# Kernel optimization log

Hardware: AMD Instinct MI355X
Metric: run time of the kernel (lower is better)

## Reference

```python
import jax, jax.numpy as jnp
import numpy as np

D_MODEL = 1024
NUM_HEADS = 16
HEAD_DIM = D_MODEL // NUM_HEADS  # 64
M_BITS = 32
B, N = 4, 2048


def setup_inputs() -> dict:
    key = jax.random.key(0)
    ks = jax.random.split(key, 6)
    s = 1.0 / np.sqrt(D_MODEL)
    se = 1.0 / np.sqrt(HEAD_DIM)
    return {
        "x": jax.random.normal(ks[0], (B, N, D_MODEL), dtype=jnp.float32),
        "Wq": jax.random.normal(ks[1], (D_MODEL, D_MODEL), dtype=jnp.float32) * s,
        "Wk": jax.random.normal(ks[2], (D_MODEL, D_MODEL), dtype=jnp.float32) * s,
        "Wv": jax.random.normal(ks[3], (D_MODEL, D_MODEL), dtype=jnp.float32) * s,
        # per-head witness (bit) encoders: project head_dim -> m_bits
        "W_enc": jax.random.normal(ks[4], (NUM_HEADS, HEAD_DIM, M_BITS), dtype=jnp.float32) * se,
        "Wo": jax.random.normal(ks[5], (D_MODEL, D_MODEL), dtype=jnp.float32) * s,
    }


def reference(x, Wq, Wk, Wv, W_enc, Wo):
    Bsz, Nq, _ = x.shape
    # QKV projections (nn.Linear, no bias): y = x @ W^T
    Q = x @ Wq.T
    K = x @ Wk.T  # self-attention: context = x
    V = x @ Wv.T
    # split heads: [B, N, H, hd]
    Qh = Q.reshape(Bsz, Nq, NUM_HEADS, HEAD_DIM)
    Kh = K.reshape(Bsz, Nq, NUM_HEADS, HEAD_DIM)
    Vh = V.reshape(Bsz, Nq, NUM_HEADS, HEAD_DIM)
    # witness encodings: soft-bit (tanh of random-hyperplane projections), m_bits << head_dim feature space
    q_enc = jnp.tanh(jnp.einsum("bnhd,hdm->bnhm", Qh, W_enc))
    k_enc = jnp.tanh(jnp.einsum("bnhd,hdm->bnhm", Kh, W_enc))
    # witness similarity scores over m_bits instead of full head_dim
    scale = 1.0 / np.sqrt(M_BITS)
    scores = jnp.einsum("bnhm,bkhm->bhnk", q_enc, k_enc) * scale  # [B,H,N,N]
    attn = jax.nn.softmax(scores, axis=-1)
    out = jnp.einsum("bhnk,bkhd->bnhd", attn, Vh).reshape(Bsz, Nq, D_MODEL)
    return out @ Wo.T
```

## Files before the change

### kernel.cpp

```cpp
#include <hip/hip_runtime.h>

typedef unsigned short u16;
typedef unsigned int u32;

typedef __bf16 bfrag __attribute__((ext_vector_type(8)));
typedef float f32x4 __attribute__((ext_vector_type(4)));
typedef float f32x16 __attribute__((ext_vector_type(16)));
typedef float f32x2 __attribute__((ext_vector_type(2)));

__device__ __forceinline__ float b2f(u16 h) {
    u32 u = ((u32)h) << 16;
    return __builtin_bit_cast(float, u);
}
__device__ __forceinline__ u16 f2b(float f) {
    u32 u = __builtin_bit_cast(u32, f);
    u += 0x7fffu + ((u >> 16) & 1u);
    return (u16)(u >> 16);
}
__device__ __forceinline__ u32 cvtpk(float lo, float hi) {
    u32 r;
    asm("v_cvt_pk_bf16_f32 %0, %1, %2" : "=v"(r) : "v"(lo), "v"(hi));
    return r;
}

#if defined(__has_builtin)
#if __has_builtin(__builtin_amdgcn_exp2f)
#define EXP2(x) __builtin_amdgcn_exp2f(x)
#endif
#endif
#ifndef EXP2
#define EXP2(x) exp2f(x)
#endif

#if defined(__has_builtin)
#if __has_builtin(__builtin_amdgcn_global_load_lds)
#define HAS_GLL 1
#endif
#endif
#ifndef HAS_GLL
#define HAS_GLL 0
#endif

#if HAS_GLL
typedef __attribute__((address_space(1))) const u32 as1_u32;
typedef __attribute__((address_space(3))) u32 as3_u32;
__device__ __forceinline__ void gl_lds16(const u16* g, u16* l) {
    __builtin_amdgcn_global_load_lds((as1_u32*)g, (as3_u32*)l, 16, 0, 0);
}
#endif

#if defined(__has_builtin)
#if __has_builtin(__builtin_amdgcn_permlane32_swap)
#define HAS_PLS 1
#endif
#endif
#ifndef HAS_PLS
#define HAS_PLS 0
#endif

__device__ __forceinline__ void plswap(u32 a, u32 b, u32& o0, u32& o1) {
#if HAS_PLS
    auto r = __builtin_amdgcn_permlane32_swap((int)a, (int)b, false, false);
    o0 = (u32)r[0];
    o1 = (u32)r[1];
#else
    int idx = ((int)(threadIdx.x & 63) ^ 32) << 2;
    u32 ca = (u32)__builtin_amdgcn_ds_bpermute(idx, (int)a);
    u32 cb = (u32)__builtin_amdgcn_ds_bpermute(idx, (int)b);
    bool hi = (threadIdx.x & 63) >= 32;
    o0 = hi ? cb : a;
    o1 = hi ? b : ca;
#endif
}

__device__ __forceinline__ void xcd_swizzle(int& bxn, int& bym) {
    int gx = gridDim.x;
    int nwg = gx * gridDim.y;
    int orig = blockIdx.x + gx * blockIdx.y;
    int nid = orig;
    if ((nwg & 7) == 0) {
        int cpx = nwg >> 3;
        nid = (orig & 7) * cpx + (orig >> 3);
    }
    bxn = nid % gx;
    bym = nid / gx;
}

#define BATCH 4
#define SEQ   2048
#define DM    1024
#define NH    16
#define HD    64
#define MB    32
#define STOK  (BATCH * SEQ)

#define QSCALE 0.25503524337503433f
#define TWOLOG2E 2.8853900817779268f

__device__ __forceinline__ void storeC(u16* C, size_t idx, float v)   { C[idx] = f2b(v); }
__device__ __forceinline__ void storeC(float* C, size_t idx, float v) { C[idx] = v; }

__global__ __launch_bounds__(256) void cvt3_f32_bf16(
    const float* __restrict__ a, const float* __restrict__ b,
    const float* __restrict__ c,
    u16* __restrict__ da, u16* __restrict__ db, u16* __restrict__ dc,
    int n8a, int n8bc)
{
    const int job = blockIdx.y;
    const float* s = (job == 0) ? a : ((job == 1) ? b : c);
    u16* d = (job == 0) ? da : ((job == 1) ? db : dc);
    int n8 = (job == 0) ? n8a : n8bc;
    int i = blockIdx.x * 256 + threadIdx.x;
    if (i >= n8) return;
    const float4* sp = (const float4*)s + (size_t)i * 2;
    float4 x = sp[0], y = sp[1];
    u16 t[8] = { f2b(x.x), f2b(x.y), f2b(x.z), f2b(x.w),
                 f2b(y.x), f2b(y.y), f2b(y.z), f2b(y.w) };
    ((uint4*)d)[i] = *(uint4*)t;
}

__global__ __launch_bounds__(256) void build_cqk(
    const float* __restrict__ Wq, const float* __restrict__ Wk,
    const float* __restrict__ Wenc, u16* __restrict__ CqkT)
{
    const int dblk = blockIdx.x;
    const int qk   = blockIdx.y >> 4;
    const int h    = blockIdx.y & 15;
    const float* W = qk ? Wk : Wq;
    __shared__ float we[64][32];
    const int tid = threadIdx.x;

    for (int p = 0; p < 8; ++p) {
        int idx = p * 256 + tid;
        we[idx >> 5][idx & 31] = Wenc[(size_t)h * (HD * MB) + idx];
    }
    __syncthreads();

    const int mh = tid >> 7;
    const int d  = dblk * 128 + (tid & 127);
    float acc[16] = {};
    for (int dh = 0; dh < 64; ++dh) {
        float w = W[(size_t)(h * 64 + dh) * DM + d];
        for (int m = 0; m < 16; ++m)
            acc[m] += w * we[dh][mh * 16 + m];
    }
    u16* dst = CqkT + (size_t)(qk * 512 + h * 32 + mh * 16) * DM + d;
    for (int m = 0; m < 16; ++m)
        dst[(size_t)m * DM] = f2b(acc[m]);
}

template <int TBM, typename TC>
__global__ __launch_bounds__(256) void gemm_bt(
    const u16* __restrict__ A, const u16* __restrict__ Bt, TC* __restrict__ C,
    int M, int Nc, int K)
{
    constexpr int FI = TBM / 32;
    __shared__ alignas(16) u16 As[TBM * 32];
    __shared__ alignas(16) u16 Bs[128 * 32];

    const int tid  = threadIdx.x;
    const int wave = tid >> 6;
    const int lane = tid & 63;
    const int quad = lane >> 4;
    const int lrow = lane & 15;
    int bxn, bym;
    xcd_swizzle(bxn, bym);
    const int bm = bym * TBM;
    const int bn = bxn * 128;
    const int wm = (wave & 1) * (TBM / 2);
    const int wn = (wave >> 1) * 64;

    f32x4 acc[FI][4] = {};

    for (int k0 = 0; k0 < K; k0 += 32) {
#if HAS_GLL
        for (int p = 0; p < TBM / 64; ++p) {
            int cbase = wave * TBM + p * 64;
            int cme   = cbase + lane;
            int row = cme >> 2, col = (cme & 3) * 8;
            gl_lds16(&A[(size_t)(bm + row) * K + k0 + col], &As[(size_t)cbase * 8]);
        }
        for (int p = 0; p < 2; ++p) {
            int cbase = wave * 128 + p * 64;
            int cme   = cbase + lane;
            int row = cme >> 2, col = (cme & 3) * 8;
            gl_lds16(&Bt[(size_t)(bn + row) * K + k0 + col], &Bs[(size_t)cbase * 8]);
        }
#else
        for (int p = 0; p < TBM / 64; ++p) {
            int idx = p * 256 + tid, row = idx >> 2, col = (idx & 3) * 8;
            *(uint4*)&As[row * 32 + col] = *(const uint4*)&A[(size_t)(bm + row) * K + k0 + col];
        }
        for (int p = 0; p < 2; ++p) {
            int idx = p * 256 + tid, row = idx >> 2, col = (idx & 3) * 8;
            *(uint4*)&Bs[row * 32 + col] = *(const uint4*)&Bt[(size_t)(bn + row) * K + k0 + col];
        }
#endif
        __syncthreads();

        bfrag af[FI], bfv[4];
        for (int i = 0; i < FI; ++i)
            af[i] = *(const bfrag*)&As[(wm + i * 16 + lrow) * 32 + quad * 8];
        for (int j = 0; j < 4; ++j)
            bfv[j] = *(const bfrag*)&Bs[(wn + j * 16 + lrow) * 32 + quad * 8];

        for (int i = 0; i < FI; ++i)
            for (int j = 0; j < 4; ++j)
                acc[i][j] = __builtin_amdgcn_mfma_f32_16x16x32_bf16(af[i], bfv[j], acc[i][j], 0, 0, 0);
        __syncthreads();
    }

    for (int i = 0; i < FI; ++i)
        for (int j = 0; j < 4; ++j)
            for (int r = 0; r < 4; ++r) {
                int row = bm + wm + i * 16 + quad * 4 + r;
                int col = bn + wn + j * 16 + lrow;
                storeC(C, (size_t)row * Nc + col, acc[i][j][r]);
            }
}

__global__ __launch_bounds__(256) void gemm_encv(
    const u16* __restrict__ A, const u16* __restrict__ Bt,
    u16* __restrict__ qe, u16* __restrict__ ke, u16* __restrict__ Vt)
{
    __shared__ alignas(16) u16 As[128 * 32];
    __shared__ alignas(16) u16 Bs[128 * 32];

    const int tid  = threadIdx.x;
    const int wave = tid >> 6;
    const int lane = tid & 63;
    const int quad = lane >> 4;
    const int lrow = lane & 15;
    int bxn, bym;
    xcd_swizzle(bxn, bym);
    const int bm = bym * 128;
    const int bn = bxn * 128;
    const int wm = (wave & 1) * 64;
    const int wn = (wave >> 1) * 64;

    f32x4 acc[4][4] = {};

    for (int k0 = 0; k0 < DM; k0 += 32) {
#if HAS_GLL
        for (int p = 0; p < 2; ++p) {
            int cbase = wave * 128 + p * 64;
            int cme   = cbase + lane;
            int row = cme >> 2, col = (cme & 3) * 8;
            gl_lds16(&A[(size_t)(bm + row) * DM + k0 + col], &As[(size_t)cbase * 8]);
            gl_lds16(&Bt[(size_t)(bn + row) * DM + k0 + col], &Bs[(size_t)cbase * 8]);
        }
#else
        for (int p = 0; p < 2; ++p) {
            int idx = p * 256 + tid, row = idx >> 2, col = (idx & 3) * 8;
            *(uint4*)&As[row * 32 + col] = *(const uint4*)&A[(size_t)(bm + row) * DM + k0 + col];
            *(uint4*)&Bs[row * 32 + col] = *(const uint4*)&Bt[(size_t)(bn + row) * DM + k0 + col];
        }
#endif
        __syncthreads();

        bfrag af[4], bfv[4];
        for (int i = 0; i < 4; ++i)
            af[i] = *(const bfrag*)&As[(wm + i * 16 + lrow) * 32 + quad * 8];
        for (int j = 0; j < 4; ++j)
            bfv[j] = *(const bfrag*)&Bs[(wn + j * 16 + lrow) * 32 + quad * 8];

        for (int i = 0; i < 4; ++i)
            for (int j = 0; j < 4; ++j)
                acc[i][j] = __builtin_amdgcn_mfma_f32_16x16x32_bf16(af[i], bfv[j], acc[i][j], 0, 0, 0);
        __syncthreads();
    }

    if (bn < 1024) {
        for (int i = 0; i < 4; ++i)
            for (int j = 0; j < 4; ++j) {
                int col = bn + wn + j * 16 + lrow;
                int hh = (col >> 5) & 15;
                int mm = col & 31;
                u16* dst = (col < 512) ? qe : ke;
                float qs = (col < 512) ? QSCALE : 1.0f;
                for (int r = 0; r < 4; ++r) {
                    int row = bm + wm + i * 16 + quad * 4 + r;
                    int bb = row >> 11, nn = row & 2047;
                    float e = EXP2(acc[i][j][r] * TWOLOG2E);
                    float t = (1.f - 2.f / (e + 1.f)) * qs;
                    dst[((size_t)(bb * NH + hh) * SEQ + nn) * MB + mm] = f2b(t);
                }
            }
    } else {
        for (int i = 0; i < 4; ++i)
            for (int j = 0; j < 4; ++j) {
                int col = bn - 1024 + wn + j * 16 + lrow;
                int hh = col >> 6, dd = col & 63;
                int row0 = bm + wm + i * 16 + quad * 4;
                int bb = row0 >> 11, nn = row0 & 2047;
                u16 t4[4] = { f2b(acc[i][j][0]), f2b(acc[i][j][1]),
                              f2b(acc[i][j][2]), f2b(acc[i][j][3]) };
                *(uint2*)&Vt[((size_t)(bb * NH + hh) * HD + dd) * SEQ + nn] = *(uint2*)t4;
            }
    }
}

__global__ __launch_bounds__(256, 4) void flash_attn(
    const u16* __restrict__ qe,
    const u16* __restrict__ ke,
    const u16* __restrict__ Vt,
    u16* __restrict__ AO)
{
    const int h = blockIdx.x, b = blockIdx.y, qt = blockIdx.z;
    const int tid  = threadIdx.x;
    const int wave = tid >> 6;
    const int lane = tid & 63;
    const int r31  = lane & 31;
    const int hi   = lane >> 5;

    __shared__ alignas(16) u16 Kt[2][64 * 32];
    __shared__ alignas(16) u16 Vtile[2][64 * 64];

    const size_t bhh = (size_t)(b * NH + h);
    const u16* keb = ke + bhh * SEQ * MB;
    const u16* qeb = qe + bhh * SEQ * MB;
    const u16* vtb = Vt + bhh * HD * SEQ;

    const int q0w = qt * 128 + wave * 32;

    const int klr = tid >> 2;
    const int ksl = tid & 3;
    const u16* ksrc = keb + (size_t)klr * MB + ((ksl ^ (klr & 3)) * 8);
    const int d0 = wave * 8 + (lane >> 3);
    const int c0 = lane & 7;
    const int g0 = (c0 ^ (d0 & 7)) * 8;
    const u16* vsrc0 = vtb + (size_t)d0 * SEQ + g0;
    const u16* vsrc1 = vtb + (size_t)(d0 + 32) * SEQ + g0;

#if HAS_GLL
    gl_lds16(ksrc,  Kt[0] + wave * 512);
    gl_lds16(vsrc0, Vtile[0] + wave * 512);
    gl_lds16(vsrc1, Vtile[0] + 2048 + wave * 512);
#else
    *(uint4*)&Kt[0][klr * 32 + ksl * 8] = *(const uint4*)ksrc;
    *(uint4*)&Vtile[0][d0 * 64 + c0 * 8] = *(const uint4*)vsrc0;
    *(uint4*)&Vtile[0][(d0 + 32) * 64 + c0 * 8] = *(const uint4*)vsrc1;
#endif
    ksrc += 64 * MB;
    vsrc0 += 64;
    vsrc1 += 64;

    bfrag qf[2];
    {
        const u16* qrow = qeb + (size_t)(q0w + r31) * MB;
        qf[0] = *(const bfrag*)&qrow[hi * 8];
        qf[1] = *(const bfrag*)&qrow[16 + hi * 8];
    }

    const f32x16 zero16 = {};

    f32x16 Oa[2] = {};
    f32x2 dacc = {0.f, 0.f};
    const int ksw = r31 & 3;
    const int vsw = r31 & 7;

    for (int c = 0; c < 32; ++c) {
        const int cur = c & 1, nxt = cur ^ 1;
        __syncthreads();

        if (c + 1 < 32) {
#if HAS_GLL
            gl_lds16(ksrc,  Kt[nxt] + wave * 512);
            gl_lds16(vsrc0, Vtile[nxt] + wave * 512);
            gl_lds16(vsrc1, Vtile[nxt] + 2048 + wave * 512);
#else
            *(uint4*)&Kt[nxt][klr * 32 + ksl * 8] = *(const uint4*)ksrc;
            *(uint4*)&Vtile[nxt][d0 * 64 + c0 * 8] = *(const uint4*)vsrc0;
            *(uint4*)&Vtile[nxt][(d0 + 32) * 64 + c0 * 8] = *(const uint4*)vsrc1;
#endif
            ksrc += 64 * MB;
            vsrc0 += 64;
            vsrc1 += 64;
        }

        const u16* KtC = Kt[cur];
        const u16* VtC = Vtile[cur];

        bfrag kf[2][2];
        for (int kt = 0; kt < 2; ++kt) {
            const u16* krow = &KtC[(kt * 32 + r31) * 32];
            kf[kt][0] = *(const bfrag*)&krow[((hi    ) ^ ksw) * 8];
            kf[kt][1] = *(const bfrag*)&krow[((2 + hi) ^ ksw) * 8];
        }

        bfrag pf[2][2];
        for (int kt = 0; kt < 2; ++kt) {
            __builtin_amdgcn_s_setprio(1);
            f32x16 St = __builtin_amdgcn_mfma_f32_32x32x16_bf16(kf[kt][0], qf[0], zero16, 0, 0, 0);
            St = __builtin_amdgcn_mfma_f32_32x32x16_bf16(kf[kt][1], qf[1], St, 0, 0, 0);
            __builtin_amdgcn_s_setprio(0);
            for (int kc = 0; kc < 2; ++kc) {
                float e0 = EXP2(St[8 * kc + 0]);
                float e1 = EXP2(St[8 * kc + 1]);
                float e2 = EXP2(St[8 * kc + 2]);
                float e3 = EXP2(St[8 * kc + 3]);
                float e4 = EXP2(St[8 * kc + 4]);
                float e5 = EXP2(St[8 * kc + 5]);
                float e6 = EXP2(St[8 * kc + 6]);
                float e7 = EXP2(St[8 * kc + 7]);
                f32x2 p0 = {e0, e1}, p1 = {e2, e3}, p2 = {e4, e5}, p3 = {e6, e7};
                dacc += (p0 + p1) + (p2 + p3);
                u32 A0 = cvtpk(e0, e1), A1 = cvtpk(e2, e3);
                u32 B0 = cvtpk(e4, e5), B1 = cvtpk(e6, e7);
                u32 w0, w1, w2, w3;
                plswap(A0, B0, w0, w2);
                plswap(A1, B1, w1, w3);
                uint4 words = { w0, w1, w2, w3 };
                pf[kt][kc] = __builtin_bit_cast(bfrag, words);
            }
        }

        __builtin_amdgcn_s_setprio(1);
        for (int dt = 0; dt < 2; ++dt) {
            const u16* vrow = &VtC[(dt * 32 + r31) * 64];
            for (int kt = 0; kt < 2; ++kt)
                for (int kc = 0; kc < 2; ++kc) {
                    bfrag vf = *(const bfrag*)&vrow[(((kt * 4 + kc * 2 + hi) ^ vsw) * 8)];
                    Oa[dt] = __builtin_amdgcn_mfma_f32_32x32x16_bf16(vf, pf[kt][kc], Oa[dt], 0, 0, 0);
                }
        }
        __builtin_amdgcn_s_setprio(0);
    }

    float dsum = dacc[0] + dacc[1];
    u32 o0, o1;
    plswap(__builtin_bit_cast(u32, dsum), __builtin_bit_cast(u32, dsum), o0, o1);
    float den = __builtin_bit_cast(float, o0) + __builtin_bit_cast(float, o1);

    {
        float inv = 1.0f / den;
        u16* aob = AO + (size_t)(b * SEQ + q0w + r31) * DM + h * HD;
        for (int dt = 0; dt < 2; ++dt)
            for (int g = 0; g < 4; ++g) {
                u16 t4[4] = { f2b(Oa[dt][g * 4 + 0] * inv),
                              f2b(Oa[dt][g * 4 + 1] * inv),
                              f2b(Oa[dt][g * 4 + 2] * inv),
                              f2b(Oa[dt][g * 4 + 3] * inv) };
                *(uint2*)&aob[dt * 32 + g * 8 + hi * 4] = *(uint2*)t4;
            }
    }
}

extern "C" void kernel_launch(void* const* d_in, const int* in_sizes, int n_in,
                              void* d_out, int out_size, void* d_ws, size_t ws_size,
                              hipStream_t stream) {
    const float* x    = (const float*)d_in[0];
    const float* Wq   = (const float*)d_in[1];
    const float* Wk   = (const float*)d_in[2];
    const float* Wv   = (const float*)d_in[3];
    const float* Wenc = (const float*)d_in[4];
    const float* Wo   = (const float*)d_in[5];
    float* out = (float*)d_out;

    const size_t MB1 = (size_t)1024 * 1024;
    char* ws = (char*)d_ws;
    u16* AO   = (u16*)(ws);
    u16* Wo_b = (u16*)(ws + 16 * MB1);
    u16* Bc   = (u16*)(ws + 18 * MB1);
    u16* Vt   = (u16*)(ws + 24 * MB1);
    u16* qe   = (u16*)(ws + 48 * MB1);
    u16* ke   = (u16*)(ws + 56 * MB1);

    u16* xb = (u16*)d_out;
    u16* wvb = Bc + (size_t)1024 * DM;

    cvt3_f32_bf16<<<dim3(STOK * DM / 8 / 256, 3), 256, 0, stream>>>(
        x, Wv, Wo, xb, wvb, Wo_b, STOK * DM / 8, DM * DM / 8);
    build_cqk<<<dim3(8, 32), 256, 0, stream>>>(Wq, Wk, Wenc, Bc);

    gemm_encv<<<dim3(2048 / 128, STOK / 128), 256, 0, stream>>>(xb, Bc, qe, ke, Vt);

    flash_attn<<<dim3(NH, BATCH, SEQ / 128), 256, 0, stream>>>(qe, ke, Vt, AO);

    gemm_bt<64, float><<<dim3(DM / 128, STOK / 64), 256, 0, stream>>>(AO, Wo_b, out, STOK, DM, DM);
}
```

Measured before the change: 251.5 us.

## Shrink flash attention blocks to two waves and 32-key tiles

Restructures the attention kernel so each block has 2 waves covering 64 queries instead of 4 waves covering 128, and iterates over 32-key chunks (64 iterations) instead of 64-key chunks. The K and V shared-memory tiles are halved and the V load/swizzle pattern now matches the K layout. The aim is lower register and LDS pressure per block, more blocks in flight, and a shorter softmax-to-MFMA dependency per iteration. The cost is twice as many barriers and K/V tile loads per query, and K/V reuse across queries within a block is halved.

```diff
diff --git a/kernel.cpp b/kernel.cpp
--- a/kernel.cpp
+++ b/kernel.cpp
@@ -300,7 +300,28 @@
     }
 }
 
-__global__ __launch_bounds__(256, 4) void flash_attn(
+__device__ __forceinline__ bfrag pack_half(const f32x16& St, int kc, f32x2& dacc)
+{
+    float e0 = EXP2(St[8 * kc + 0]);
+    float e1 = EXP2(St[8 * kc + 1]);
+    float e2 = EXP2(St[8 * kc + 2]);
+    float e3 = EXP2(St[8 * kc + 3]);
+    float e4 = EXP2(St[8 * kc + 4]);
+    float e5 = EXP2(St[8 * kc + 5]);
+    float e6 = EXP2(St[8 * kc + 6]);
+    float e7 = EXP2(St[8 * kc + 7]);
+    f32x2 p0 = {e0, e1}, p1 = {e2, e3}, p2 = {e4, e5}, p3 = {e6, e7};
+    dacc += (p0 + p1) + (p2 + p3);
+    u32 A0 = cvtpk(e0, e1), A1 = cvtpk(e2, e3);
+    u32 B0 = cvtpk(e4, e5), B1 = cvtpk(e6, e7);
+    u32 w0, w1, w2, w3;
+    plswap(A0, B0, w0, w2);
+    plswap(A1, B1, w1, w3);
+    uint4 words = { w0, w1, w2, w3 };
+    return __builtin_bit_cast(bfrag, words);
+}
+
+__global__ __launch_bounds__(128, 4) void flash_attn(
     const u16* __restrict__ qe,
     const u16* __restrict__ ke,
     const u16* __restrict__ Vt,
@@ -313,116 +334,95 @@
     const int r31  = lane & 31;
     const int hi   = lane >> 5;
 
-    __shared__ alignas(16) u16 Kt[2][64 * 32];
-    __shared__ alignas(16) u16 Vtile[2][64 * 64];
+    __shared__ alignas(16) u16 Kt[2][32 * 32];
+    __shared__ alignas(16) u16 Vtile[2][64 * 32];
 
     const size_t bhh = (size_t)(b * NH + h);
     const u16* keb = ke + bhh * SEQ * MB;
     const u16* qeb = qe + bhh * SEQ * MB;
     const u16* vtb = Vt + bhh * HD * SEQ;
 
-    const int q0w = qt * 128 + wave * 32;
+    const int q0w = qt * 64 + wave * 32;
 
     const int klr = tid >> 2;
     const int ksl = tid & 3;
     const u16* ksrc = keb + (size_t)klr * MB + ((ksl ^ (klr & 3)) * 8);
-    const int d0 = wave * 8 + (lane >> 3);
-    const int c0 = lane & 7;
-    const int g0 = (c0 ^ (d0 & 7)) * 8;
-    const u16* vsrc0 = vtb + (size_t)d0 * SEQ + g0;
-    const u16* vsrc1 = vtb + (size_t)(d0 + 32) * SEQ + g0;
+    const u16* vsrc0 = vtb + (size_t)klr * SEQ + ((ksl ^ (klr & 3)) * 8);
+    const u16* vsrc1 = vtb + (size_t)(klr + 32) * SEQ + ((ksl ^ (klr & 3)) * 8);
 
 #if HAS_GLL
     gl_lds16(ksrc,  Kt[0] + wave * 512);
     gl_lds16(vsrc0, Vtile[0] + wave * 512);
-    gl_lds16(vsrc1, Vtile[0] + 2048 + wave * 512);
+    gl_lds16(vsrc1, Vtile[0] + 1024 + wave * 512);
 #else
     *(uint4*)&Kt[0][klr * 32 + ksl * 8] = *(const uint4*)ksrc;
-    *(uint4*)&Vtile[0][d0 * 64 + c0 * 8] = *(const uint4*)vsrc0;
-    *(uint4*)&Vtile[0][(d0 + 32) * 64 + c0 * 8] = *(const uint4*)vsrc1;
-#endif
-    ksrc += 64 * MB;
-    vsrc0 += 64;
-    vsrc1 += 64;
-
-    bfrag qf[2];
+    *(uint4*)&Vtile[0][klr * 32 + ksl * 8] = *(const uint4*)vsrc0;
+    *(uint4*)&Vtile[0][(klr + 32) * 32 + ksl * 8] = *(const uint4*)vsrc1;
+#endif
+    ksrc += 32 * MB;
+    vsrc0 += 32;
+    vsrc1 += 32;
+
+    bfrag qf0, qf1;
     {
         const u16* qrow = qeb + (size_t)(q0w + r31) * MB;
-        qf[0] = *(const bfrag*)&qrow[hi * 8];
-        qf[1] = *(const bfrag*)&qrow[16 + hi * 8];
+        qf0 = *(const bfrag*)&qrow[hi * 8];
+        qf1 = *(const bfrag*)&qrow[16 + hi * 8];
     }
 
     const f32x16 zero16 = {};
 
-    f32x16 Oa[2] = {};
+    f32x16 Oa0 = {}, Oa1 = {};
     f32x2 dacc = {0.f, 0.f};
-    const int ksw = r31 & 3;
-    const int vsw = r31 & 7;
-
-    for (int c = 0; c < 32; ++c) {
+    const int sw = r31 & 3;
+
+    for (int c = 0; c < 64; ++c) {
         const int cur = c & 1, nxt = cur ^ 1;
         __syncthreads();
 
-        if (c + 1 < 32) {
+        if (c + 1 < 64) {
 #if HAS_GLL
             gl_lds16(ksrc,  Kt[nxt] + wave * 512);
             gl_lds16(vsrc0, Vtile[nxt] + wave * 512);
-            gl_lds16(vsrc1, Vtile[nxt] + 2048 + wave * 512);
+            gl_lds16(vsrc1, Vtile[nxt] + 1024 + wave * 512);
 #else
             *(uint4*)&Kt[nxt][klr * 32 + ksl * 8] = *(const uint4*)ksrc;
-            *(uint4*)&Vtile[nxt][d0 * 64 + c0 * 8] = *(const uint4*)vsrc0;
-            *(uint4*)&Vtile[nxt][(d0 + 32) * 64 + c0 * 8] = *(const uint4*)vsrc1;
-#endif
-            ksrc += 64 * MB;
-            vsrc0 += 64;
-            vsrc1 += 64;
+            *(uint4*)&Vtile[nxt][klr * 32 + ksl * 8] = *(const uint4*)vsrc0;
+            *(uint4*)&Vtile[nxt][(klr + 32) * 32 + ksl * 8] = *(const uint4*)vsrc1;
+#endif
+            ksrc += 32 * MB;
+            vsrc0 += 32;
+            vsrc1 += 32;
         }
 
         const u16* KtC = Kt[cur];
         const u16* VtC = Vtile[cur];
 
-        bfrag kf[2][2];
-        for (int kt = 0; kt < 2; ++kt) {
-            const u16* krow = &KtC[(kt * 32 + r31) * 32];
-            kf[kt][0] = *(const bfrag*)&krow[((hi    ) ^ ksw) * 8];
-            kf[kt][1] = *(const bfrag*)&krow[((2 + hi) ^ ksw) * 8];
-        }
-
-        bfrag pf[2][2];
-        for (int kt = 0; kt < 2; ++kt) {
-            __builtin_amdgcn_s_setprio(1);
-            f32x16 St = __builtin_amdgcn_mfma_f32_32x32x16_bf16(kf[kt][0], qf[0], zero16, 0, 0, 0);
-            St = __builtin_amdgcn_mfma_f32_32x32x16_bf16(kf[kt][1], qf[1], St, 0, 0, 0);
-            __builtin_amdgcn_s_setprio(0);
-            for (int kc = 0; kc < 2; ++kc) {
-                float e0 = EXP2(St[8 * kc + 0]);
-                float e1 = EXP2(St[8 * kc + 1]);
-                float e2 = EXP2(St[8 * kc + 2]);
-                float e3 = EXP2(St[8 * kc + 3]);
-                float e4 = EXP2(St[8 * kc + 4]);
-                float e5 = EXP2(St[8 * kc + 5]);
-                float e6 = EXP2(St[8 * kc + 6]);
-                float e7 = EXP2(St[8 * kc + 7]);
-                f32x2 p0 = {e0, e1}, p1 = {e2, e3}, p2 = {e4, e5}, p3 = {e6, e7};
-                dacc += (p0 + p1) + (p2 + p3);
-                u32 A0 = cvtpk(e0, e1), A1 = cvtpk(e2, e3);
-                u32 B0 = cvtpk(e4, e5), B1 = cvtpk(e6, e7);
-                u32 w0, w1, w2, w3;
-                plswap(A0, B0, w0, w2);
-                plswap(A1, B1, w1, w3);
-                uint4 words = { w0, w1, w2, w3 };
-                pf[kt][kc] = __builtin_bit_cast(bfrag, words);
-            }
-        }
+        const u16* krow = &KtC[r31 * 32];
+        bfrag kf0 = *(const bfrag*)&krow[((hi    ) ^ sw) * 8];
+        bfrag kf1 = *(const bfrag*)&krow[((2 + hi) ^ sw) * 8];
 
         __builtin_amdgcn_s_setprio(1);
-        for (int dt = 0; dt < 2; ++dt) {
-            const u16* vrow = &VtC[(dt * 32 + r31) * 64];
-            for (int kt = 0; kt < 2; ++kt)
-                for (int kc = 0; kc < 2; ++kc) {
-                    bfrag vf = *(const bfrag*)&vrow[(((kt * 4 + kc * 2 + hi) ^ vsw) * 8)];
-                    Oa[dt] = __builtin_amdgcn_mfma_f32_32x32x16_bf16(vf, pf[kt][kc], Oa[dt], 0, 0, 0);
-                }
+        f32x16 St = __builtin_amdgcn_mfma_f32_32x32x16_bf16(kf0, qf0, zero16, 0, 0, 0);
+        St = __builtin_amdgcn_mfma_f32_32x32x16_bf16(kf1, qf1, St, 0, 0, 0);
+        __builtin_amdgcn_s_setprio(0);
+        bfrag pf0 = pack_half(St, 0, dacc);
+        bfrag pf1 = pack_half(St, 1, dacc);
+
+        __builtin_amdgcn_s_setprio(1);
+        const u16* vrow0 = &VtC[(size_t)r31 * 32];
+        const u16* vrow1 = &VtC[(size_t)(32 + r31) * 32];
+        {
+            int ch0 = ((hi    ) ^ sw) * 8;
+            int ch1 = ((2 + hi) ^ sw) * 8;
+            bfrag v00 = *(const bfrag*)&vrow0[ch0];
+            bfrag v01 = *(const bfrag*)&vrow0[ch1];
+            bfrag v10 = *(const bfrag*)&vrow1[ch0];
+            bfrag v11 = *(const bfrag*)&vrow1[ch1];
+            Oa0 = __builtin_amdgcn_mfma_f32_32x32x16_bf16(v00, pf0, Oa0, 0, 0, 0);
+            Oa0 = __builtin_amdgcn_mfma_f32_32x32x16_bf16(v01, pf1, Oa0, 0, 0, 0);
+            Oa1 = __builtin_amdgcn_mfma_f32_32x32x16_bf16(v10, pf0, Oa1, 0, 0, 0);
+            Oa1 = __builtin_amdgcn_mfma_f32_32x32x16_bf16(v11, pf1, Oa1, 0, 0, 0);
         }
         __builtin_amdgcn_s_setprio(0);
     }
@@ -435,14 +435,16 @@
     {
         float inv = 1.0f / den;
         u16* aob = AO + (size_t)(b * SEQ + q0w + r31) * DM + h * HD;
-        for (int dt = 0; dt < 2; ++dt)
-            for (int g = 0; g < 4; ++g) {
-                u16 t4[4] = { f2b(Oa[dt][g * 4 + 0] * inv),
-                              f2b(Oa[dt][g * 4 + 1] * inv),
-                              f2b(Oa[dt][g * 4 + 2] * inv),
-                              f2b(Oa[dt][g * 4 + 3] * inv) };
-                *(uint2*)&aob[dt * 32 + g * 8 + hi * 4] = *(uint2*)t4;
-            }
+        for (int g = 0; g < 4; ++g) {
+            u16 t4[4] = { f2b(Oa0[g * 4 + 0] * inv), f2b(Oa0[g * 4 + 1] * inv),
+                          f2b(Oa0[g * 4 + 2] * inv), f2b(Oa0[g * 4 + 3] * inv) };
+            *(uint2*)&aob[g * 8 + hi * 4] = *(uint2*)t4;
+        }
+        for (int g = 0; g < 4; ++g) {
+            u16 t4[4] = { f2b(Oa1[g * 4 + 0] * inv), f2b(Oa1[g * 4 + 1] * inv),
+                          f2b(Oa1[g * 4 + 2] * inv), f2b(Oa1[g * 4 + 3] * inv) };
+            *(uint2*)&aob[32 + g * 8 + hi * 4] = *(uint2*)t4;
+        }
     }
 }
 
@@ -475,7 +477,7 @@
 
     gemm_encv<<<dim3(2048 / 128, STOK / 128), 256, 0, stream>>>(xb, Bc, qe, ke, Vt);
 
-    flash_attn<<<dim3(NH, BATCH, SEQ / 128), 256, 0, stream>>>(qe, ke, Vt, AO);
+    flash_attn<<<dim3(NH, BATCH, SEQ / 64), 128, 0, stream>>>(qe, ke, Vt, AO);
 
     gemm_bt<64, float><<<dim3(DM / 128, STOK / 64), 256, 0, stream>>>(AO, Wo_b, out, STOK, DM, DM);
 }
```

Measured after the change: 263.1 us. 4.6% more time.
